# Optimization experiments

Hardware: AMD Instinct MI355X
Metric: run time of the kernel (lower is better)

## Reference

```python
import jax, jax.numpy as jnp
import numpy as np

# Static module config (must match init_kwargs / input_specs)
C, HEADS, POINTS, LEVELS = 256, 8, 8, 2
H, W = 128, 128           # BEV grid per agent/level
NQ = H * W                # num_query = H*W
DH = C // HEADS           # per-head dim


def setup_inputs() -> dict:
    key = jax.random.key(0)
    ks = jax.random.split(key, 12)
    s = 0.02
    return {
        "query": jax.random.normal(ks[0], (1, NQ, C), jnp.float32),
        "query_pos": jax.random.normal(ks[1], (1, NQ, C), jnp.float32),
        "value": jax.random.normal(ks[2], (LEVELS, NQ, C), jnp.float32),
        "reference_points": jax.random.uniform(ks[3], (1, NQ, LEVELS, 2), jnp.float32),
        "spatial_shapes": jnp.full((LEVELS, 2), H, dtype=jnp.int32),
        "W_off": jax.random.normal(ks[4], (C, LEVELS * HEADS * POINTS * 2), jnp.float32) * s,
        "b_off": jax.random.normal(ks[5], (LEVELS * HEADS * POINTS * 2,), jnp.float32) * s,
        "W_attn": jax.random.normal(ks[6], (C, LEVELS * HEADS * POINTS), jnp.float32) * s,
        "b_attn": jax.random.normal(ks[7], (LEVELS * HEADS * POINTS,), jnp.float32) * s,
        "W_val": jax.random.normal(ks[8], (C, C), jnp.float32) * s,
        "b_val": jax.random.normal(ks[9], (C,), jnp.float32) * s,
        "W_out": jax.random.normal(ks[10], (C, C), jnp.float32) * s,
        "b_out": jax.random.normal(ks[11], (C,), jnp.float32) * s,
    }


def _bilinear(img, x, y):
    """grid_sample-style bilinear, align_corners=False, zero padding.
    img: (H, W, D); x, y: (...) pixel-space coords. Returns (..., D)."""
    Hh, Ww = img.shape[0], img.shape[1]
    x0f, y0f = jnp.floor(x), jnp.floor(y)
    x0, y0 = x0f.astype(jnp.int32), y0f.astype(jnp.int32)
    x1, y1 = x0 + 1, y0 + 1
    wx1, wy1 = x - x0f, y - y0f
    wx0, wy0 = 1.0 - wx1, 1.0 - wy1

    def gather(yy, xx):
        valid = (yy >= 0) & (yy < Hh) & (xx >= 0) & (xx < Ww)
        g = img[jnp.clip(yy, 0, Hh - 1), jnp.clip(xx, 0, Ww - 1)]
        return jnp.where(valid[..., None], g, 0.0)

    return (gather(y0, x0) * (wy0 * wx0)[..., None]
            + gather(y0, x1) * (wy0 * wx1)[..., None]
            + gather(y1, x0) * (wy1 * wx0)[..., None]
            + gather(y1, x1) * (wy1 * wx1)[..., None])


_sample_heads = jax.vmap(_bilinear, in_axes=(0, 0, 0))  # over heads


def reference(query, query_pos, value, reference_points, spatial_shapes,
              W_off, b_off, W_attn, b_attn, W_val, b_val, W_out, b_out):
    identity = query                                        # (1, NQ, C)
    q = (query + query_pos)[0]                              # (NQ, C), bs=1

    v = value @ W_val + b_val                               # (L, NQ, C)
    v = v.reshape(LEVELS, H, W, HEADS, DH)                  # per-level feature maps

    off = (q @ W_off + b_off).reshape(NQ, HEADS, LEVELS, POINTS, 2)
    attn = (q @ W_attn + b_attn).reshape(NQ, HEADS, LEVELS * POINTS)
    attn = jax.nn.softmax(attn, axis=-1).reshape(NQ, HEADS, LEVELS, POINTS)

    # offset_normalizer = (W, H) per level
    norm = jnp.stack([spatial_shapes[:, 1], spatial_shapes[:, 0]], -1).astype(q.dtype)  # (L, 2)
    # sampling_locations in normalized [0,1] coords: (NQ, HEADS, LEVELS, POINTS, 2)
    loc = reference_points[0][:, None, :, None, :] + off / norm[None, None, :, None, :]

    out = jnp.zeros((NQ, HEADS, DH), dtype=q.dtype)
    for l in range(LEVELS):
        img_l = jnp.transpose(v[l], (2, 0, 1, 3))           # (HEADS, H, W, DH)
        # align_corners=False: px = x_norm * W - 0.5
        xl = jnp.transpose(loc[:, :, l, :, 0], (1, 0, 2)) * W - 0.5  # (HEADS, NQ, POINTS)
        yl = jnp.transpose(loc[:, :, l, :, 1], (1, 0, 2)) * H - 0.5
        sampled = _sample_heads(img_l, xl, yl)              # (HEADS, NQ, POINTS, DH)
        out = out + jnp.einsum('hqpd,qhp->qhd', sampled, attn[:, :, l, :])

    out = out.reshape(NQ, C) @ W_out + b_out                # (NQ, C)
    return out[None] + identity                             # dropout is identity (eval / p=0)
```

## Files before the change

kernel.cpp:

```cpp
#include <hip/hip_runtime.h>
#include <hip/hip_bf16.h>
#include <math.h>

#define NQ     16384
#define CDIM   256
#define NHEADS 8
#define NPTS   8
#define NLVL   2
#define HH     128
#define WWID   128
#define DHEAD  32
#define NCAT   384

#define PW        130
#define CELLB     32
#define ROWB      (PW * CELLB)
#define MAPB      (PW * PW * CELLB)
#define BORDER_BLKS 16
#define TRANS_BLKS  224

typedef __bf16 bf16_t;
typedef __bf16 bf16x8 __attribute__((ext_vector_type(8)));
typedef float  f32x4  __attribute__((ext_vector_type(4)));
typedef float  f32x2  __attribute__((ext_vector_type(2)));

typedef __attribute__((address_space(1))) const uint32_t gau32;
typedef __attribute__((address_space(3))) uint32_t lau32;

__device__ __forceinline__ bf16_t f2b(float f) { return (bf16_t)f; }

__device__ __forceinline__ bf16x8 cvt8(float4 a, float4 b) {
    bf16x8 v;
    v[0] = f2b(a.x); v[1] = f2b(a.y); v[2] = f2b(a.z); v[3] = f2b(a.w);
    v[4] = f2b(b.x); v[5] = f2b(b.y); v[6] = f2b(b.z); v[7] = f2b(b.w);
    return v;
}

__global__ __launch_bounds__(256) void prep_k(const float* __restrict__ W_val,
                                              const float* __restrict__ W_off,
                                              const float* __restrict__ W_attn,
                                              const float* __restrict__ W_out,
                                              unsigned char* __restrict__ v2,
                                              bf16_t* __restrict__ Wt_val,
                                              bf16_t* __restrict__ Wt_qa,
                                              bf16_t* __restrict__ Wt_out) {
    const int b = blockIdx.x;
    if (b < BORDER_BLKS) {
        unsigned char* map = v2 + (size_t)b * MAPB;
        for (int i = threadIdx.x; i < 516; i += 256) {
            int y, x;
            if (i < 130)      { y = 0;        x = i;       }
            else if (i < 260) { y = 129;      x = i - 130; }
            else if (i < 388) { y = i - 259;  x = 0;       }
            else              { y = i - 387;  x = 129;     }
            uint4* p = reinterpret_cast<uint4*>(map + (size_t)y * ROWB + x * CELLB);
            p[0] = make_uint4(0, 0, 0, 0);
            p[1] = make_uint4(0, 0, 0, 0);
        }
        return;
    }
    {
        const int tb = b - BORDER_BLKS;
        const float* W; bf16_t* Wt; int N, t; bool permute = false;
        if (tb < 64)       { W = W_val;  Wt = Wt_val;            N = 256; t = tb;       permute = true; }
        else if (tb < 128) { W = W_off;  Wt = Wt_qa;             N = 256; t = tb - 64;  }
        else if (tb < 160) { W = W_attn; Wt = Wt_qa + 256 * 256; N = 128; t = tb - 128; }
        else               { W = W_out;  Wt = Wt_out;            N = 256; t = tb - 160; }
        const int ntn = N >> 5;
        const int k0 = (t / ntn) * 32, n0 = (t % ntn) * 32;
        const int tx = threadIdx.x & 31, ty = threadIdx.x >> 5;
        __shared__ float s[32][33];
#pragma unroll
        for (int i = 0; i < 4; ++i)
            s[ty + 8 * i][tx] = W[(size_t)(k0 + ty + 8 * i) * N + n0 + tx];
        __syncthreads();
#pragma unroll
        for (int i = 0; i < 4; ++i) {
            const int n = n0 + ty + 8 * i;
            const int p = permute ? ((n & ~63) | ((n & 3) << 4) | ((n & 63) >> 2)) : n;
            Wt[(size_t)p * 256 + k0 + tx] = f2b(s[tx][ty + 8 * i]);
        }
    }
}

template <int AMODE, bool OUT_BF16, bool ADD_SRC, bool PERM_V>
__device__ __forceinline__ void gemm_body(bf16_t (&As)[2][128][64], bf16_t (&Bs)[2][128][64],
                                          int bidx, int bidy,
                                          const bf16_t* __restrict__ Abf,
                                          const float* __restrict__ Af0,
                                          const float* __restrict__ Af1,
                                          const bf16_t* __restrict__ Bt,
                                          const float* __restrict__ bias,
                                          const float* __restrict__ bias2,
                                          int Nsplit,
                                          const float* __restrict__ addsrc,
                                          void* __restrict__ Cout,
                                          int N, int K) {
    const int tid  = threadIdx.x;
    const int wave = tid >> 6;
    const int lane = tid & 63;
    const int rowBase = bidy * 128;
    const int colBase = bidx * 128;
    const int wm = (wave & 1) * 64;
    const int wn = (wave >> 1) * 64;
    const int fr = lane & 15;
    const int fq = lane >> 4;

    f32x4 acc[4][4] = {};

    const int lrow = lane >> 3;
    const int scol = ((lane & 7) ^ lrow) * 8;
    const int nt = K >> 6;

    float4 ra[4][2], rb[4][2];

    auto issueA = [&](int t, int buf) {
        if constexpr (AMODE == 0) {
#pragma unroll
            for (int tt = 0; tt < 4; ++tt) {
                const bf16_t* src =
                    Abf + (size_t)(rowBase + wave * 32 + tt * 8 + lrow) * K + t * 64 + scol;
                __builtin_amdgcn_global_load_lds((gau32*)src,
                                                 (lau32*)&As[buf][wave * 32 + tt * 8][0],
                                                 16, 0, 0);
            }
        } else {
#pragma unroll
            for (int tt = 0; tt < 4; ++tt) {
                const float* src =
                    Af0 + (size_t)(rowBase + wave * 32 + tt * 8 + lrow) * K + t * 64 + scol;
                ra[tt][0] = *reinterpret_cast<const float4*>(src);
                ra[tt][1] = *reinterpret_cast<const float4*>(src + 4);
            }
            if constexpr (AMODE == 2) {
#pragma unroll
                for (int tt = 0; tt < 4; ++tt) {
                    const float* src =
                        Af1 + (size_t)(rowBase + wave * 32 + tt * 8 + lrow) * K + t * 64 + scol;
                    rb[tt][0] = *reinterpret_cast<const float4*>(src);
                    rb[tt][1] = *reinterpret_cast<const float4*>(src + 4);
                }
            }
        }
    };
    auto issueB = [&](int t, int buf) {
#pragma unroll
        for (int tt = 0; tt < 4; ++tt) {
            const bf16_t* src =
                Bt + (size_t)(colBase + wave * 32 + tt * 8 + lrow) * K + t * 64 + scol;
            __builtin_amdgcn_global_load_lds((gau32*)src,
                                             (lau32*)&Bs[buf][wave * 32 + tt * 8][0],
                                             16, 0, 0);
        }
    };
    auto writeA = [&](int buf) {
        if constexpr (AMODE != 0) {
#pragma unroll
            for (int tt = 0; tt < 4; ++tt) {
                float4 a = ra[tt][0], c = ra[tt][1];
                if constexpr (AMODE == 2) {
                    a.x += rb[tt][0].x; a.y += rb[tt][0].y;
                    a.z += rb[tt][0].z; a.w += rb[tt][0].w;
                    c.x += rb[tt][1].x; c.y += rb[tt][1].y;
                    c.z += rb[tt][1].z; c.w += rb[tt][1].w;
                }
                *reinterpret_cast<bf16x8*>(
                    &As[buf][wave * 32 + tt * 8 + lrow][(lane & 7) * 8]) = cvt8(a, c);
            }
        }
    };

    issueA(0, 0);
    issueB(0, 0);
    writeA(0);
    __syncthreads();

    for (int t = 0; t < nt; ++t) {
        const int c = t & 1, n = c ^ 1;
        if (t + 1 < nt) {
            issueA(t + 1, n);
            issueB(t + 1, n);
        }
#pragma unroll
        for (int ks = 0; ks < 2; ++ks) {
            const int gk = ((ks * 4 + fq) ^ (fr & 7)) * 8;
            bf16x8 af[4], bfr[4];
#pragma unroll
            for (int i = 0; i < 4; ++i)
                af[i] = *reinterpret_cast<const bf16x8*>(&As[c][wm + i * 16 + fr][gk]);
#pragma unroll
            for (int j = 0; j < 4; ++j)
                bfr[j] = *reinterpret_cast<const bf16x8*>(&Bs[c][wn + j * 16 + fr][gk]);
#pragma unroll
            for (int i = 0; i < 4; ++i)
#pragma unroll
                for (int j = 0; j < 4; ++j)
                    acc[i][j] = __builtin_amdgcn_mfma_f32_16x16x32_bf16(af[i], bfr[j],
                                                                        acc[i][j], 0, 0, 0);
        }
        if (t + 1 < nt) {
            writeA(n);
            __syncthreads();
        }
    }

    if (PERM_V) {
        const int lbase = colBase + wn + fr * 4;
        const float bv0 = bias[lbase], bv1 = bias[lbase + 1];
        const float bv2 = bias[lbase + 2], bv3 = bias[lbase + 3];
        const int hh = (lbase >> 5) & 7;
        const int dbase = lbase & 31;
        unsigned char* outp = (unsigned char*)Cout;
#pragma unroll
        for (int i = 0; i < 4; ++i) {
#pragma unroll
            for (int r = 0; r < 4; ++r) {
                const int row = rowBase + wm + i * 16 + fq * 4 + r;
                const int lv = row >> 14, cell = row & 16383;
                const int y = cell >> 7, x = cell & 127;
                uint32_t pk = __builtin_amdgcn_cvt_pk_fp8_f32(
                    acc[i][0][r] + bv0, acc[i][1][r] + bv1, 0, false);
                pk = (uint32_t)__builtin_amdgcn_cvt_pk_fp8_f32(
                    acc[i][2][r] + bv2, acc[i][3][r] + bv3, pk, true);
                *reinterpret_cast<uint32_t*>(
                    outp + (size_t)(lv * NHEADS + hh) * MAPB
                         + (size_t)(y + 1) * ROWB + (x + 1) * CELLB + dbase) = pk;
            }
        }
        return;
    }

#pragma unroll
    for (int j = 0; j < 4; ++j) {
        const int col = colBase + wn + j * 16 + fr;
        const float bv = (col < Nsplit) ? bias[col] : bias2[col - Nsplit];
#pragma unroll
        for (int i = 0; i < 4; ++i) {
#pragma unroll
            for (int r = 0; r < 4; ++r) {
                const int row = rowBase + wm + i * 16 + fq * 4 + r;
                float vv = acc[i][j][r] + bv;
                if (ADD_SRC) vv += addsrc[(size_t)row * N + col];
                if (OUT_BF16)
                    ((bf16_t*)Cout)[(size_t)row * N + col] = f2b(vv);
                else
                    ((float*)Cout)[(size_t)row * N + col] = vv;
            }
        }
    }
}

__global__ __launch_bounds__(256, 2) void fused_proj_k(const float* __restrict__ value,
                                                       const float* __restrict__ query,
                                                       const float* __restrict__ query_pos,
                                                       const bf16_t* __restrict__ Wt_val,
                                                       const bf16_t* __restrict__ Wt_qa,
                                                       const float* __restrict__ b_val,
                                                       const float* __restrict__ b_off,
                                                       const float* __restrict__ b_attn,
                                                       unsigned char* __restrict__ v2,
                                                       bf16_t* __restrict__ cbuf) {
    __shared__ __align__(16) bf16_t As[2][128][64];
    __shared__ __align__(16) bf16_t Bs[2][128][64];
    const int b = blockIdx.x;
    if (b < 512) {
        const int bidy = (b >> 4) * 8 + (b & 7);
        const int bidx = (b >> 3) & 1;
        gemm_body<1, true, false, true>(As, Bs, bidx, bidy, nullptr, value, nullptr,
                                        Wt_val, b_val, b_val, 256, nullptr, v2,
                                        CDIM, CDIM);
    } else {
        const int b2 = b - 512;
        const int bidy = (b2 / 24) * 8 + (b2 & 7);
        const int bidx = (b2 >> 3) % 3;
        gemm_body<2, true, false, false>(As, Bs, bidx, bidy, nullptr, query, query_pos,
                                         Wt_qa, b_off, b_attn, 256, nullptr, cbuf,
                                         NCAT, CDIM);
    }
}

__global__ __launch_bounds__(256, 2) void outproj_k(const bf16_t* __restrict__ tmp,
                                                    const bf16_t* __restrict__ Wt_out,
                                                    const float* __restrict__ b_out,
                                                    const float* __restrict__ query,
                                                    float* __restrict__ out) {
    __shared__ __align__(16) bf16_t As[2][128][64];
    __shared__ __align__(16) bf16_t Bs[2][128][64];
    const int b = blockIdx.x;
    const int bidy = (b >> 4) * 8 + (b & 7);
    const int bidx = (b >> 3) & 1;
    gemm_body<0, false, true, false>(As, Bs, bidx, bidy, tmp, nullptr, nullptr,
                                     Wt_out, b_out, b_out, 256, query, out,
                                     CDIM, CDIM);
}

__device__ __forceinline__ void acc_tap4(uint4 u, float w, f32x2* acc2) {
    acc2[0] += __builtin_amdgcn_cvt_pk_f32_fp8((int)u.x, false) * w;
    acc2[1] += __builtin_amdgcn_cvt_pk_f32_fp8((int)u.x, true)  * w;
    acc2[2] += __builtin_amdgcn_cvt_pk_f32_fp8((int)u.y, false) * w;
    acc2[3] += __builtin_amdgcn_cvt_pk_f32_fp8((int)u.y, true)  * w;
    acc2[4] += __builtin_amdgcn_cvt_pk_f32_fp8((int)u.z, false) * w;
    acc2[5] += __builtin_amdgcn_cvt_pk_f32_fp8((int)u.z, true)  * w;
    acc2[6] += __builtin_amdgcn_cvt_pk_f32_fp8((int)u.w, false) * w;
    acc2[7] += __builtin_amdgcn_cvt_pk_f32_fp8((int)u.w, true)  * w;
}

__global__ __launch_bounds__(256) void sample_k(const unsigned char* __restrict__ v2,
                                                const bf16_t* __restrict__ cbuf,
                                                const float* __restrict__ refp,
                                                bf16_t* __restrict__ tmp) {
    const int b    = blockIdx.x;
    const int h    = b & 7;
    const int qblk = b >> 3;
    const int tid  = threadIdx.x;
    const int qloc = tid >> 1;
    const int ck   = tid & 1;
    const int q    = qblk * 128 + qloc;

    const bf16_t* qrow = cbuf + (size_t)q * NCAT;
    const float4 rp = *reinterpret_cast<const float4*>(refp + (size_t)q * 4);

    const bf16_t* attp = qrow + 256 + h * 16;
    bf16x8 A0 = *reinterpret_cast<const bf16x8*>(attp);
    bf16x8 A1 = *reinterpret_cast<const bf16x8*>(attp + 8);
    float e[16];
#pragma unroll
    for (int i = 0; i < 8; ++i) { e[i] = (float)A0[i]; e[8 + i] = (float)A1[i]; }
    float m = e[0];
#pragma unroll
    for (int i = 1; i < 16; ++i) m = fmaxf(m, e[i]);
    float s = 0.f;
#pragma unroll
    for (int i = 0; i < 16; ++i) { e[i] = __expf(e[i] - m); s += e[i]; }
    const float inv = 1.f / s;
#pragma unroll
    for (int i = 0; i < 16; ++i) e[i] *= inv;

    f32x2 acc2[8] = {};

#pragma unroll
    for (int l = 0; l < NLVL; ++l) {
        const float bx = (l == 0 ? rp.x : rp.z) * (float)WWID - 0.5f;
        const float by = (l == 0 ? rp.y : rp.w) * (float)HH - 0.5f;
        const unsigned char* base = v2 + (size_t)(l * NHEADS + h) * MAPB
                                       + 131 * CELLB + ck * 16;
        const bf16_t* offp = qrow + h * 32 + l * 16;
        bf16x8 o0 = *reinterpret_cast<const bf16x8*>(offp);
        bf16x8 o1 = *reinterpret_cast<const bf16x8*>(offp + 8);
        float ox[8], oy[8];
#pragma unroll
        for (int i = 0; i < 4; ++i) {
            ox[i]     = (float)o0[2 * i];  oy[i]     = (float)o0[2 * i + 1];
            ox[4 + i] = (float)o1[2 * i];  oy[4 + i] = (float)o1[2 * i + 1];
        }

#pragma unroll
        for (int p = 0; p < NPTS; ++p) {
            const float px = bx + ox[p];
            const float py = by + oy[p];
            const float w  = e[l * 8 + p];
            const float x0f = floorf(px), y0f = floorf(py);
            const int x0 = (int)x0f, y0 = (int)y0f;
            const float wx1 = px - x0f, wy1 = py - y0f;
            const float wx0 = 1.f - wx1, wy0 = 1.f - wy1;
            const int x0c = min(max(x0, -1), 128);
            const int x1c = min(max(x0 + 1, -1), 128);
            const int y0c = min(max(y0, -1), 128);
            const int y1c = min(max(y0 + 1, -1), 128);
            const unsigned char* r0 = base + y0c * ROWB;
            const unsigned char* r1 = base + y1c * ROWB;
            uint4 u00 = *reinterpret_cast<const uint4*>(r0 + x0c * CELLB);
            uint4 u10 = *reinterpret_cast<const uint4*>(r0 + x1c * CELLB);
            uint4 u01 = *reinterpret_cast<const uint4*>(r1 + x0c * CELLB);
            uint4 u11 = *reinterpret_cast<const uint4*>(r1 + x1c * CELLB);
            const float wy0w = w * wy0, wy1w = w * wy1;
            acc_tap4(u00, wy0w * wx0, acc2);
            acc_tap4(u10, wy0w * wx1, acc2);
            acc_tap4(u01, wy1w * wx0, acc2);
            acc_tap4(u11, wy1w * wx1, acc2);
        }
    }

    bf16x8 ov0, ov1;
#pragma unroll
    for (int i = 0; i < 4; ++i) {
        ov0[2 * i]     = f2b(acc2[i].x);
        ov0[2 * i + 1] = f2b(acc2[i].y);
        ov1[2 * i]     = f2b(acc2[4 + i].x);
        ov1[2 * i + 1] = f2b(acc2[4 + i].y);
    }
    bf16_t* op = tmp + (size_t)q * CDIM + h * DHEAD + ck * 16;
    *reinterpret_cast<bf16x8*>(op)     = ov0;
    *reinterpret_cast<bf16x8*>(op + 8) = ov1;
}

extern "C" void kernel_launch(void* const* d_in, const int* in_sizes, int n_in,
                              void* d_out, int out_size, void* d_ws, size_t ws_size,
                              hipStream_t stream) {
    const float* query     = (const float*)d_in[0];
    const float* query_pos = (const float*)d_in[1];
    const float* value     = (const float*)d_in[2];
    const float* refp      = (const float*)d_in[3];
    const float* W_off  = (const float*)d_in[5];
    const float* b_off  = (const float*)d_in[6];
    const float* W_attn = (const float*)d_in[7];
    const float* b_attn = (const float*)d_in[8];
    const float* W_val  = (const float*)d_in[9];
    const float* b_val  = (const float*)d_in[10];
    const float* W_out  = (const float*)d_in[11];
    const float* b_out  = (const float*)d_in[12];
    float* out = (float*)d_out;

    char* ws = (char*)d_ws;
    unsigned char* v2 = (unsigned char*)(ws);
    bf16_t* cbuf    = (bf16_t*)(ws + 8654848);
    bf16_t* tmp     = (bf16_t*)(ws + 21237760);
    bf16_t* Wt_val  = (bf16_t*)(ws + 29626368);
    bf16_t* Wt_qa   = (bf16_t*)(ws + 29757440);
    bf16_t* Wt_out  = (bf16_t*)(ws + 29954048);

    prep_k<<<BORDER_BLKS + TRANS_BLKS, 256, 0, stream>>>(
        W_val, W_off, W_attn, W_out, v2, Wt_val, Wt_qa, Wt_out);
    fused_proj_k<<<896, 256, 0, stream>>>(value, query, query_pos,
                                          Wt_val, Wt_qa, b_val, b_off, b_attn,
                                          v2, cbuf);
    sample_k<<<1024, 256, 0, stream>>>(v2, cbuf, refp, tmp);
    outproj_k<<<256, 256, 0, stream>>>(tmp, Wt_out, b_out, query, out);
}
```

Before: 177.8 us.

## Split sampling across four threads per query and retile output projection to 64x64

The sampling kernel now assigns four threads per query-head, each covering 8 channels with 8-byte fp8 loads instead of 16. This doubles the grid, cuts per-thread registers, and adds an occupancy hint of 8 blocks. The output projection is replaced by a dedicated 64x64-tile MFMA GEMM with swizzled LDS staging and 1024 blocks, so it fills more CUs. The cost is more per-thread softmax and coordinate work repeated across the extra threads, plus smaller load granules.

```diff
diff --git a/kernel.cpp b/kernel.cpp
--- a/kernel.cpp
+++ b/kernel.cpp
@@ -279,43 +279,99 @@
     }
 }
 
-__global__ __launch_bounds__(256, 2) void outproj_k(const bf16_t* __restrict__ tmp,
+__global__ __launch_bounds__(256, 4) void outproj_k(const bf16_t* __restrict__ tmp,
                                                     const bf16_t* __restrict__ Wt_out,
                                                     const float* __restrict__ b_out,
                                                     const float* __restrict__ query,
                                                     float* __restrict__ out) {
-    __shared__ __align__(16) bf16_t As[2][128][64];
-    __shared__ __align__(16) bf16_t Bs[2][128][64];
+    __shared__ __align__(16) bf16_t As[2][64][64];
+    __shared__ __align__(16) bf16_t Bs[2][64][64];
     const int b = blockIdx.x;
-    const int bidy = (b >> 4) * 8 + (b & 7);
-    const int bidx = (b >> 3) & 1;
-    gemm_body<0, false, true, false>(As, Bs, bidx, bidy, tmp, nullptr, nullptr,
-                                     Wt_out, b_out, b_out, 256, query, out,
-                                     CDIM, CDIM);
-}
-
-__device__ __forceinline__ void acc_tap4(uint4 u, float w, f32x2* acc2) {
+    const int bidy = b >> 2, bidx = b & 3;
+    const int tid = threadIdx.x, wave = tid >> 6, lane = tid & 63;
+    const int rowBase = bidy * 64, colBase = bidx * 64;
+    const int wm = (wave & 1) * 32, wn = (wave >> 1) * 32;
+    const int fr = lane & 15, fq = lane >> 4;
+    const int lrow = lane >> 3;
+    const int K = 256;
+
+    f32x4 acc[2][2] = {};
+
+    auto stage = [&](int t, int buf) {
+#pragma unroll
+        for (int p = 0; p < 2; ++p) {
+            const int row = wave * 16 + p * 8 + lrow;
+            const int s = ((lane & 7) ^ (row & 7)) * 8;
+            const bf16_t* srcA = tmp + (size_t)(rowBase + row) * K + t * 64 + s;
+            __builtin_amdgcn_global_load_lds((gau32*)srcA,
+                                             (lau32*)&As[buf][wave * 16 + p * 8][0],
+                                             16, 0, 0);
+            const bf16_t* srcB = Wt_out + (size_t)(colBase + row) * K + t * 64 + s;
+            __builtin_amdgcn_global_load_lds((gau32*)srcB,
+                                             (lau32*)&Bs[buf][wave * 16 + p * 8][0],
+                                             16, 0, 0);
+        }
+    };
+
+    stage(0, 0);
+    __syncthreads();
+    for (int t = 0; t < 4; ++t) {
+        const int c = t & 1, n = c ^ 1;
+        if (t + 1 < 4) stage(t + 1, n);
+#pragma unroll
+        for (int ks = 0; ks < 2; ++ks) {
+            const int gk = ((ks * 4 + fq) ^ (fr & 7)) * 8;
+            bf16x8 af[2], bfr[2];
+#pragma unroll
+            for (int i = 0; i < 2; ++i)
+                af[i] = *reinterpret_cast<const bf16x8*>(&As[c][wm + i * 16 + fr][gk]);
+#pragma unroll
+            for (int j = 0; j < 2; ++j)
+                bfr[j] = *reinterpret_cast<const bf16x8*>(&Bs[c][wn + j * 16 + fr][gk]);
+#pragma unroll
+            for (int i = 0; i < 2; ++i)
+#pragma unroll
+                for (int j = 0; j < 2; ++j)
+                    acc[i][j] = __builtin_amdgcn_mfma_f32_16x16x32_bf16(af[i], bfr[j],
+                                                                        acc[i][j], 0, 0, 0);
+        }
+        if (t + 1 < 4) __syncthreads();
+    }
+
+#pragma unroll
+    for (int j = 0; j < 2; ++j) {
+        const int col = colBase + wn + j * 16 + fr;
+        const float bv = b_out[col];
+#pragma unroll
+        for (int i = 0; i < 2; ++i) {
+#pragma unroll
+            for (int r = 0; r < 4; ++r) {
+                const int row = rowBase + wm + i * 16 + fq * 4 + r;
+                out[(size_t)row * CDIM + col] =
+                    acc[i][j][r] + bv + query[(size_t)row * CDIM + col];
+            }
+        }
+    }
+}
+
+__device__ __forceinline__ void acc_tap2(uint2 u, float w, f32x2* acc2) {
     acc2[0] += __builtin_amdgcn_cvt_pk_f32_fp8((int)u.x, false) * w;
     acc2[1] += __builtin_amdgcn_cvt_pk_f32_fp8((int)u.x, true)  * w;
     acc2[2] += __builtin_amdgcn_cvt_pk_f32_fp8((int)u.y, false) * w;
     acc2[3] += __builtin_amdgcn_cvt_pk_f32_fp8((int)u.y, true)  * w;
-    acc2[4] += __builtin_amdgcn_cvt_pk_f32_fp8((int)u.z, false) * w;
-    acc2[5] += __builtin_amdgcn_cvt_pk_f32_fp8((int)u.z, true)  * w;
-    acc2[6] += __builtin_amdgcn_cvt_pk_f32_fp8((int)u.w, false) * w;
-    acc2[7] += __builtin_amdgcn_cvt_pk_f32_fp8((int)u.w, true)  * w;
-}
-
-__global__ __launch_bounds__(256) void sample_k(const unsigned char* __restrict__ v2,
-                                                const bf16_t* __restrict__ cbuf,
-                                                const float* __restrict__ refp,
-                                                bf16_t* __restrict__ tmp) {
+}
+
+__global__ __launch_bounds__(256, 8) void sample_k(const unsigned char* __restrict__ v2,
+                                                   const bf16_t* __restrict__ cbuf,
+                                                   const float* __restrict__ refp,
+                                                   bf16_t* __restrict__ tmp) {
     const int b    = blockIdx.x;
     const int h    = b & 7;
     const int qblk = b >> 3;
     const int tid  = threadIdx.x;
-    const int qloc = tid >> 1;
-    const int ck   = tid & 1;
-    const int q    = qblk * 128 + qloc;
+    const int qloc = tid >> 2;
+    const int ck   = tid & 3;
+    const int q    = qblk * 64 + qloc;
 
     const bf16_t* qrow = cbuf + (size_t)q * NCAT;
     const float4 rp = *reinterpret_cast<const float4*>(refp + (size_t)q * 4);
@@ -336,14 +392,14 @@
 #pragma unroll
     for (int i = 0; i < 16; ++i) e[i] *= inv;
 
-    f32x2 acc2[8] = {};
+    f32x2 acc2[4] = {};
 
 #pragma unroll
     for (int l = 0; l < NLVL; ++l) {
         const float bx = (l == 0 ? rp.x : rp.z) * (float)WWID - 0.5f;
         const float by = (l == 0 ? rp.y : rp.w) * (float)HH - 0.5f;
         const unsigned char* base = v2 + (size_t)(l * NHEADS + h) * MAPB
-                                       + 131 * CELLB + ck * 16;
+                                       + 131 * CELLB + ck * 8;
         const bf16_t* offp = qrow + h * 32 + l * 16;
         bf16x8 o0 = *reinterpret_cast<const bf16x8*>(offp);
         bf16x8 o1 = *reinterpret_cast<const bf16x8*>(offp + 8);
@@ -369,29 +425,26 @@
             const int y1c = min(max(y0 + 1, -1), 128);
             const unsigned char* r0 = base + y0c * ROWB;
             const unsigned char* r1 = base + y1c * ROWB;
-            uint4 u00 = *reinterpret_cast<const uint4*>(r0 + x0c * CELLB);
-            uint4 u10 = *reinterpret_cast<const uint4*>(r0 + x1c * CELLB);
-            uint4 u01 = *reinterpret_cast<const uint4*>(r1 + x0c * CELLB);
-            uint4 u11 = *reinterpret_cast<const uint4*>(r1 + x1c * CELLB);
+            uint2 u00 = *reinterpret_cast<const uint2*>(r0 + x0c * CELLB);
+            uint2 u10 = *reinterpret_cast<const uint2*>(r0 + x1c * CELLB);
+            uint2 u01 = *reinterpret_cast<const uint2*>(r1 + x0c * CELLB);
+            uint2 u11 = *reinterpret_cast<const uint2*>(r1 + x1c * CELLB);
             const float wy0w = w * wy0, wy1w = w * wy1;
-            acc_tap4(u00, wy0w * wx0, acc2);
-            acc_tap4(u10, wy0w * wx1, acc2);
-            acc_tap4(u01, wy1w * wx0, acc2);
-            acc_tap4(u11, wy1w * wx1, acc2);
-        }
-    }
-
-    bf16x8 ov0, ov1;
+            acc_tap2(u00, wy0w * wx0, acc2);
+            acc_tap2(u10, wy0w * wx1, acc2);
+            acc_tap2(u01, wy1w * wx0, acc2);
+            acc_tap2(u11, wy1w * wx1, acc2);
+        }
+    }
+
+    bf16x8 ov;
 #pragma unroll
     for (int i = 0; i < 4; ++i) {
-        ov0[2 * i]     = f2b(acc2[i].x);
-        ov0[2 * i + 1] = f2b(acc2[i].y);
-        ov1[2 * i]     = f2b(acc2[4 + i].x);
-        ov1[2 * i + 1] = f2b(acc2[4 + i].y);
-    }
-    bf16_t* op = tmp + (size_t)q * CDIM + h * DHEAD + ck * 16;
-    *reinterpret_cast<bf16x8*>(op)     = ov0;
-    *reinterpret_cast<bf16x8*>(op + 8) = ov1;
+        ov[2 * i]     = f2b(acc2[i].x);
+        ov[2 * i + 1] = f2b(acc2[i].y);
+    }
+    bf16_t* op = tmp + (size_t)q * CDIM + h * DHEAD + ck * 8;
+    *reinterpret_cast<bf16x8*>(op) = ov;
 }
 
 extern "C" void kernel_launch(void* const* d_in, const int* in_sizes, int n_in,
@@ -424,6 +477,6 @@
     fused_proj_k<<<896, 256, 0, stream>>>(value, query, query_pos,
                                           Wt_val, Wt_qa, b_val, b_off, b_attn,
                                           v2, cbuf);
-    sample_k<<<1024, 256, 0, stream>>>(v2, cbuf, refp, tmp);
-    outproj_k<<<256, 256, 0, stream>>>(tmp, Wt_out, b_out, query, out);
-}
+    sample_k<<<2048, 256, 0, stream>>>(v2, cbuf, refp, tmp);
+    outproj_k<<<1024, 256, 0, stream>>>(tmp, Wt_out, b_out, query, out);
+}
```

Measured after the change: 175.6 us, median of 2. About the same (-1.3%).

## Use 64x64 tile GEMM for output projection and remap blocks per XCD

Applied to the files above, without the earlier changes.

Adds a 64x64-tile GEMM body and uses it for the output projection, so it launches 1024 blocks instead of 256 and fills more compute units on the GPU. Block-to-tile mapping in both the fused projection and the output projection is changed to interleave by blockIdx mod 8. This appears intended to give each XCD a contiguous range of tiles for better L2 locality. Smaller tiles mean less reuse per block and more redundant loads of weights and activations.

```diff
diff --git a/kernel.cpp b/kernel.cpp
--- a/kernel.cpp
+++ b/kernel.cpp
@@ -250,6 +250,82 @@
     }
 }
 
+template <int AMODE, bool OUT_BF16, bool ADD_SRC>
+__device__ __forceinline__ void gemm64_body(bf16_t (&As)[2][64][64], bf16_t (&Bs)[2][64][64],
+                                            int bidx, int bidy,
+                                            const bf16_t* __restrict__ Abf,
+                                            const bf16_t* __restrict__ Bt,
+                                            const float* __restrict__ bias,
+                                            const float* __restrict__ addsrc,
+                                            void* __restrict__ Cout,
+                                            int N, int K) {
+    const int tid  = threadIdx.x;
+    const int wave = tid >> 6;
+    const int lane = tid & 63;
+    const int rowBase = bidy * 64;
+    const int colBase = bidx * 64;
+    const int fr = lane & 15;
+    const int fq = lane >> 4;
+    const int lrow = lane >> 3;
+    const int scol = ((lane & 7) ^ lrow) * 8;
+    const int nt = K >> 6;
+
+    f32x4 acc[4] = {};
+
+    auto stage = [&](int t, int buf) {
+#pragma unroll
+        for (int p = 0; p < 2; ++p) {
+            const bf16_t* srcA =
+                Abf + (size_t)(rowBase + wave * 16 + p * 8 + lrow) * K + t * 64 + scol;
+            __builtin_amdgcn_global_load_lds((gau32*)srcA,
+                                             (lau32*)&As[buf][wave * 16 + p * 8][0],
+                                             16, 0, 0);
+            const bf16_t* srcB =
+                Bt + (size_t)(colBase + wave * 16 + p * 8 + lrow) * K + t * 64 + scol;
+            __builtin_amdgcn_global_load_lds((gau32*)srcB,
+                                             (lau32*)&Bs[buf][wave * 16 + p * 8][0],
+                                             16, 0, 0);
+        }
+    };
+
+    stage(0, 0);
+    __syncthreads();
+    for (int t = 0; t < nt; ++t) {
+        const int c = t & 1, n = c ^ 1;
+        if (t + 1 < nt) stage(t + 1, n);
+#pragma unroll
+        for (int ks = 0; ks < 2; ++ks) {
+            const int gk = ((ks * 4 + fq) ^ (fr & 7)) * 8;
+            bf16x8 af = *reinterpret_cast<const bf16x8*>(&As[c][wave * 16 + fr][gk]);
+            bf16x8 bfr[4];
+#pragma unroll
+            for (int j = 0; j < 4; ++j)
+                bfr[j] = *reinterpret_cast<const bf16x8*>(&Bs[c][j * 16 + fr][gk]);
+#pragma unroll
+            for (int j = 0; j < 4; ++j)
+                acc[j] = __builtin_amdgcn_mfma_f32_16x16x32_bf16(af, bfr[j],
+                                                                 acc[j], 0, 0, 0);
+        }
+        if (t + 1 < nt) __syncthreads();
+    }
+
+#pragma unroll
+    for (int j = 0; j < 4; ++j) {
+        const int col = colBase + j * 16 + fr;
+        const float bv = bias[col];
+#pragma unroll
+        for (int r = 0; r < 4; ++r) {
+            const int row = rowBase + wave * 16 + fq * 4 + r;
+            float vv = acc[j][r] + bv;
+            if (ADD_SRC) vv += addsrc[(size_t)row * N + col];
+            if (OUT_BF16)
+                ((bf16_t*)Cout)[(size_t)row * N + col] = f2b(vv);
+            else
+                ((float*)Cout)[(size_t)row * N + col] = vv;
+        }
+    }
+}
+
 __global__ __launch_bounds__(256, 2) void fused_proj_k(const float* __restrict__ value,
                                                        const float* __restrict__ query,
                                                        const float* __restrict__ query_pos,
@@ -264,34 +340,36 @@
     __shared__ __align__(16) bf16_t Bs[2][128][64];
     const int b = blockIdx.x;
     if (b < 512) {
-        const int bidy = (b >> 4) * 8 + (b & 7);
-        const int bidx = (b >> 3) & 1;
+        const int w = (b & 7) * 64 + (b >> 3);
+        const int bidy = w >> 1;
+        const int bidx = w & 1;
         gemm_body<1, true, false, true>(As, Bs, bidx, bidy, nullptr, value, nullptr,
                                         Wt_val, b_val, b_val, 256, nullptr, v2,
                                         CDIM, CDIM);
     } else {
         const int b2 = b - 512;
-        const int bidy = (b2 / 24) * 8 + (b2 & 7);
-        const int bidx = (b2 >> 3) % 3;
+        const int w = (b2 & 7) * 48 + (b2 >> 3);
+        const int bidy = w / 3;
+        const int bidx = w % 3;
         gemm_body<2, true, false, false>(As, Bs, bidx, bidy, nullptr, query, query_pos,
                                          Wt_qa, b_off, b_attn, 256, nullptr, cbuf,
                                          NCAT, CDIM);
     }
 }
 
-__global__ __launch_bounds__(256, 2) void outproj_k(const bf16_t* __restrict__ tmp,
+__global__ __launch_bounds__(256, 4) void outproj_k(const bf16_t* __restrict__ tmp,
                                                     const bf16_t* __restrict__ Wt_out,
                                                     const float* __restrict__ b_out,
                                                     const float* __restrict__ query,
                                                     float* __restrict__ out) {
-    __shared__ __align__(16) bf16_t As[2][128][64];
-    __shared__ __align__(16) bf16_t Bs[2][128][64];
+    __shared__ __align__(16) bf16_t As[2][64][64];
+    __shared__ __align__(16) bf16_t Bs[2][64][64];
     const int b = blockIdx.x;
-    const int bidy = (b >> 4) * 8 + (b & 7);
-    const int bidx = (b >> 3) & 1;
-    gemm_body<0, false, true, false>(As, Bs, bidx, bidy, tmp, nullptr, nullptr,
-                                     Wt_out, b_out, b_out, 256, query, out,
-                                     CDIM, CDIM);
+    const int w = (b & 7) * 128 + (b >> 3);
+    const int bidy = w >> 2;
+    const int bidx = w & 3;
+    gemm64_body<0, false, true>(As, Bs, bidx, bidy, tmp,
+                                Wt_out, b_out, query, out, CDIM, CDIM);
 }
 
 __device__ __forceinline__ void acc_tap4(uint4 u, float w, f32x2* acc2) {
@@ -425,5 +503,5 @@
                                           Wt_val, Wt_qa, b_val, b_off, b_attn,
                                           v2, cbuf);
     sample_k<<<1024, 256, 0, stream>>>(v2, cbuf, refp, tmp);
-    outproj_k<<<256, 256, 0, stream>>>(tmp, Wt_out, b_out, query, out);
-}
+    outproj_k<<<1024, 256, 0, stream>>>(tmp, Wt_out, b_out, query, out);
+}
```

After: 182.6 us. +2.7%, slower.
